# Kernel tuning notes

Measured on AMD Instinct MI355X. Metric: run time of the kernel, lower is better.

Reference implementation:

```python
import jax, jax.numpy as jnp
import numpy as np

B, T, D = 2, 2048, 2048
H, DH, DR, DL = 16, 128, 64, 512
WINDOW, STRIDE, GLOBAL = 512, 64, 128
BASE, MAX_SEQ, ORIG_MAX = 10000.0, 131072, 4096
BETA_FAST, BETA_SLOW = 32.0, 1.0
SCALE = 1.0 / np.sqrt(DH)
SCALE_ROPE = 1.0 / np.sqrt(DR)


def _yarn_inv_freq():
    base_inv = 1.0 / (BASE ** (np.arange(0, DR, 2, dtype=np.float32) / DR))
    scale = MAX_SEQ / ORIG_MAX
    freqs = np.arange(DR // 2, dtype=np.float32)
    ramp = np.clip((freqs - BETA_SLOW) / (BETA_FAST - BETA_SLOW), 0.0, 1.0)
    return jnp.asarray(base_inv * (1 - ramp) + (base_inv / scale) * ramp)

_INV_FREQ = _yarn_inv_freq()
_YARN_FACTOR = np.float32(0.1 * np.log(MAX_SEQ / ORIG_MAX) + 1.0)


def _apply_rope(x):
    # x: [B, H, T, DR]
    t = jnp.arange(x.shape[2], dtype=jnp.float32)
    fr = t[:, None] * _INV_FREQ[None, :]            # [T, DR/2]
    emb = jnp.concatenate([fr, fr], axis=-1)        # [T, DR]
    cos, sin = jnp.cos(emb), jnp.sin(emb)
    x1, x2 = jnp.split(x, 2, axis=-1)
    rot = jnp.concatenate([-x2, x1], axis=-1)
    return (x * cos + rot * sin) * _YARN_FACTOR


def _sparse_mask(seq_len):
    pos = jnp.arange(seq_len)
    qp, kp = pos[:, None], pos[None, :]
    dist = qp - kp
    half = WINDOW // 2
    window = (dist >= -half) & (dist <= half)
    dilated = (kp % STRIDE == 0) | (kp < GLOBAL)
    causal = kp <= qp
    return (window | dilated) & causal              # [T, T] bool


def setup_inputs() -> dict:
    key = jax.random.key(0)
    ks = jax.random.split(key, 9)
    s = 0.02
    return {
        "x": jax.random.normal(ks[0], (B, T, D), jnp.float32),
        "w_q": jax.random.normal(ks[1], (D, D), jnp.float32) * s,
        "w_dkv": jax.random.normal(ks[2], (D, DL), jnp.float32) * s,
        "w_uk": jax.random.normal(ks[3], (DL, D), jnp.float32) * s,
        "w_uv": jax.random.normal(ks[4], (DL, D), jnp.float32) * s,
        "w_q_pos": jax.random.normal(ks[5], (D, H * DR), jnp.float32) * s,
        "w_k_pos": jax.random.normal(ks[6], (D, H * DR), jnp.float32) * s,
        "w_o": jax.random.normal(ks[7], (D, D), jnp.float32) * s,
    }


def reference(x, w_q, w_dkv, w_uk, w_uv, w_q_pos, w_k_pos, w_o):
    b, t, _ = x.shape
    # MLA projections
    q_c = (x @ w_q).reshape(b, t, H, DH).transpose(0, 2, 1, 3)      # [B,H,T,DH]
    c_kv = x @ w_dkv                                                # [B,T,DL]
    k_c = (c_kv @ w_uk).reshape(b, t, H, DH).transpose(0, 2, 1, 3)
    v_c = (c_kv @ w_uv).reshape(b, t, H, DH).transpose(0, 2, 1, 3)
    # decoupled RoPE branch (YaRN)
    q_r = (x @ w_q_pos).reshape(b, t, H, DR).transpose(0, 2, 1, 3)
    k_r = (x @ w_k_pos).reshape(b, t, H, DR).transpose(0, 2, 1, 3)
    q_r = _apply_rope(q_r)
    k_r = _apply_rope(k_r)
    # combined content + positional scores
    scores = jnp.einsum("bhqd,bhkd->bhqk", q_c, k_c) * SCALE \
           + jnp.einsum("bhqr,bhkr->bhqk", q_r, k_r) * SCALE_ROPE
    mask = _sparse_mask(t)                                          # [T,T]
    scores = jnp.where(mask[None, None], scores, -jnp.inf)
    attn = jax.nn.softmax(scores, axis=-1)
    out = jnp.einsum("bhqk,bhkd->bhqd", attn, v_c)                  # [B,H,T,DH]
    out = out.transpose(0, 2, 1, 3).reshape(b, t, D)
    return out @ w_o
```

## Files before the change

kernel.cpp:

```cpp
#include <hip/hip_runtime.h>
#include <hip/hip_bf16.h>
#include <cstdint>

typedef __attribute__((ext_vector_type(8))) short short8_t;
typedef __attribute__((ext_vector_type(4))) short short4_t;
typedef __attribute__((ext_vector_type(4))) float f32x4_t;

#define AS1 __attribute__((address_space(1)))
#define AS3 __attribute__((address_space(3)))

__device__ __forceinline__ void gload_lds16(const void* g, void* l) {
  __builtin_amdgcn_global_load_lds((const AS1 void*)g, (AS3 void*)l, 16, 0, 0);
}

__device__ __forceinline__ short8_t ld8(const __hip_bfloat16* p) {
  return *(const short8_t*)p;
}

__global__ __launch_bounds__(256) void k_prep(
    const float* __restrict__ x, __hip_bfloat16* __restrict__ xb,
    const float* __restrict__ wq,  const float* __restrict__ wqp,
    const float* __restrict__ wkp, const float* __restrict__ wdkv,
    const float* __restrict__ wuk, const float* __restrict__ wuv,
    const float* __restrict__ wo,
    __hip_bfloat16* __restrict__ Bt1, __hip_bfloat16* __restrict__ Bt2,
    __hip_bfloat16* __restrict__ woT) {
  __shared__ float t[64][65];
  int bid = blockIdx.x;
  if (bid < 4096) {
    int i = (bid * 256 + threadIdx.x) * 8;
    union { short8_t v; __hip_bfloat16 h[8]; } u;
#pragma unroll
    for (int j = 0; j < 8; ++j) u.h[j] = __float2bfloat16(x[i + j]);
    *(short8_t*)(xb + i) = u.v;
    return;
  }
  bid -= 4096;
  const float* in; __hip_bfloat16* out; int R, C, tile;
  if (bid < 1024)      { in = wq;   out = Bt1;                 R = 2048; C = 2048; tile = bid; }
  else if (bid < 1536) { in = wqp;  out = Bt1 + 2048UL * 2048; R = 2048; C = 1024; tile = bid - 1024; }
  else if (bid < 2048) { in = wkp;  out = Bt1 + 3072UL * 2048; R = 2048; C = 1024; tile = bid - 1536; }
  else if (bid < 2304) { in = wdkv; out = Bt1 + 4096UL * 2048; R = 2048; C = 512;  tile = bid - 2048; }
  else if (bid < 2560) { in = wuk;  out = Bt2;                 R = 512;  C = 2048; tile = bid - 2304; }
  else if (bid < 2816) { in = wuv;  out = Bt2 + 2048UL * 512;  R = 512;  C = 2048; tile = bid - 2560; }
  else                 { in = wo;   out = woT;                 R = 2048; C = 2048; tile = bid - 2816; }
  int nct = C >> 6;
  int ct = tile % nct, rt = tile / nct;
  int r0 = rt << 6, c0 = ct << 6;
#pragma unroll
  for (int i = 0; i < 16; ++i) {
    int idx = i * 256 + threadIdx.x;
    int r = idx >> 6, c = idx & 63;
    t[r][c] = in[(size_t)(r0 + r) * C + c0 + c];
  }
  __syncthreads();
#pragma unroll
  for (int i = 0; i < 16; ++i) {
    int idx = i * 256 + threadIdx.x;
    int c = idx >> 6, r = idx & 63;
    out[(size_t)(c0 + c) * R + r0 + r] = __float2bfloat16(t[r][c]);
  }
}

template<int MODE>
__global__ __launch_bounds__(256) void k_gemm2(const __hip_bfloat16* __restrict__ A,
                                               const __hip_bfloat16* __restrict__ Bt,
                                               int K, int nbx,
                                               void* __restrict__ O0, void* __restrict__ O1,
                                               void* __restrict__ O2, void* __restrict__ O3,
                                               float alpha) {
  __shared__ __align__(16) __hip_bfloat16 Al[3][128 * 32];
  __shared__ __align__(16) __hip_bfloat16 Bl[3][128 * 32];
  int bx = blockIdx.x % nbx, by = blockIdx.x / nbx;
  int tid = threadIdx.x, lane = tid & 63, w = tid >> 6;
  int L = lane & 15, hi = lane >> 4;
  int wr = (w >> 1) << 6, wc = (w & 1) << 6;
  f32x4_t acc[4][4] = {};
  const __hip_bfloat16* Ag = A + (size_t)(by * 128) * K;
  const __hip_bfloat16* Bg = Bt + (size_t)(bx * 128) * K;
  int rA = w * 16 + (lane >> 2);
  int cA = ((lane & 3) ^ ((lane >> 3) & 3)) * 8;
  int NT = K >> 5;

  auto stage = [&](int s) {
    int j = s % 3;
    int k0 = s << 5;
    gload_lds16(Ag + (size_t)rA * K + k0 + cA,        &Al[j][(w * 16) * 32]);
    gload_lds16(Ag + (size_t)(rA + 64) * K + k0 + cA, &Al[j][(64 + w * 16) * 32]);
    gload_lds16(Bg + (size_t)rA * K + k0 + cA,        &Bl[j][(w * 16) * 32]);
    gload_lds16(Bg + (size_t)(rA + 64) * K + k0 + cA, &Bl[j][(64 + w * 16) * 32]);
  };

  stage(0); stage(1);
  asm volatile("s_waitcnt vmcnt(4)\ns_barrier" ::: "memory");

  int hs = hi ^ ((L >> 1) & 3);
  for (int t = 0; t < NT; ++t) {
    int j = t % 3;
    short8_t af[4], bf[4];
#pragma unroll
    for (int m = 0; m < 4; ++m) af[m] = ld8(&Al[j][(wr + 16 * m + L) * 32 + 8 * hs]);
#pragma unroll
    for (int n = 0; n < 4; ++n) bf[n] = ld8(&Bl[j][(wc + 16 * n + L) * 32 + 8 * hs]);
    if (t + 2 < NT) stage(t + 2);
    __builtin_amdgcn_s_setprio(1);
#pragma unroll
    for (int m = 0; m < 4; ++m)
#pragma unroll
      for (int n = 0; n < 4; ++n)
        acc[m][n] = __builtin_amdgcn_mfma_f32_16x16x32_bf16(af[m], bf[n], acc[m][n], 0, 0, 0);
    __builtin_amdgcn_s_setprio(0);
    if (t + 2 < NT)      asm volatile("s_waitcnt vmcnt(4)\ns_barrier" ::: "memory");
    else if (t + 1 < NT) asm volatile("s_waitcnt vmcnt(0)\ns_barrier" ::: "memory");
  }

  int r0 = by * 128 + wr + 4 * hi;
  int cb = bx * 128 + wc;

  if (MODE == 1) {
    float* C = (float*)O0;
    size_t N = (size_t)nbx << 7;
#pragma unroll
    for (int m = 0; m < 4; ++m)
#pragma unroll
      for (int n = 0; n < 4; ++n)
#pragma unroll
        for (int i = 0; i < 4; ++i)
          C[(size_t)(r0 + 16 * m + i) * N + cb + 16 * n + L] = acc[m][n][i] * alpha;
  } else if (MODE == 2) {
    __hip_bfloat16* qcb = (__hip_bfloat16*)O0;
    __hip_bfloat16* qrb = (__hip_bfloat16*)O1;
    __hip_bfloat16* krb = (__hip_bfloat16*)O2;
    __hip_bfloat16* ckv = (__hip_bfloat16*)O3;
    if (bx < 16) {
      const float SCALE = 0.08838834764831845f;
#pragma unroll
      for (int m = 0; m < 4; ++m)
#pragma unroll
        for (int n = 0; n < 4; ++n)
#pragma unroll
          for (int i = 0; i < 4; ++i)
            qcb[(size_t)(r0 + 16 * m + i) * 2048 + cb + 16 * n + L] =
                __float2bfloat16(acc[m][n][i] * SCALE);
    } else if (bx < 32) {
      bool isq = bx < 24;
      __hip_bfloat16* dst = isq ? qrb : krb;
      float osc = isq ? 0.16832169878499666f : 1.3465735902799727f;
      int cbl = cb - (isq ? 2048 : 3072);
      float invf[2];
#pragma unroll
      for (int p = 0; p < 2; ++p) {
        float fi = (float)(16 * p + L);
        float bi = __expf(fi * -0.28782313662425574f);
        float ramp = fminf(fmaxf((fi - 1.0f) * (1.0f / 31.0f), 0.0f), 1.0f);
        invf[p] = bi * (1.0f - ramp * (31.0f / 32.0f));
      }
#pragma unroll
      for (int m = 0; m < 4; ++m)
#pragma unroll
        for (int i = 0; i < 4; ++i) {
          int row = r0 + 16 * m + i;
          float ft = (float)(row & 2047);
#pragma unroll
          for (int p = 0; p < 2; ++p) {
            float sn, cs;
            __sincosf(ft * invf[p], &sn, &cs);
            float x1 = acc[m][p][i], x2 = acc[m][p + 2][i];
            dst[(size_t)row * 1024 + cbl + 16 * p + L] =
                __float2bfloat16((x1 * cs - x2 * sn) * osc);
            dst[(size_t)row * 1024 + cbl + 32 + 16 * p + L] =
                __float2bfloat16((x2 * cs + x1 * sn) * osc);
          }
        }
    } else {
      int cbl = cb - 4096;
#pragma unroll
      for (int m = 0; m < 4; ++m)
#pragma unroll
        for (int n = 0; n < 4; ++n)
#pragma unroll
          for (int i = 0; i < 4; ++i)
            ckv[(size_t)(r0 + 16 * m + i) * 512 + cbl + 16 * n + L] =
                __float2bfloat16(acc[m][n][i]);
    }
  } else if (MODE == 3) {
    __hip_bfloat16* kcb = (__hip_bfloat16*)O0;
    __hip_bfloat16* vcb = (__hip_bfloat16*)O1;
    __hip_bfloat16* vT  = (__hip_bfloat16*)O2;
    if (bx < 16) {
#pragma unroll
      for (int m = 0; m < 4; ++m)
#pragma unroll
        for (int n = 0; n < 4; ++n)
#pragma unroll
          for (int i = 0; i < 4; ++i)
            kcb[(size_t)(r0 + 16 * m + i) * 2048 + cb + 16 * n + L] =
                __float2bfloat16(acc[m][n][i]);
    } else {
#pragma unroll
      for (int m = 0; m < 4; ++m)
#pragma unroll
        for (int n = 0; n < 4; ++n) {
          int vcol = cb - 2048 + 16 * n + L;
          int hh = vcol >> 7, dh = vcol & 127;
          int row0 = r0 + 16 * m;
          int b = row0 >> 11, t0 = row0 & 2047;
          union { short4_t v; __hip_bfloat16 h4[4]; } pk;
#pragma unroll
          for (int i = 0; i < 4; ++i) {
            __hip_bfloat16 bv = __float2bfloat16(acc[m][n][i]);
            vcb[(size_t)(row0 + i) * 2048 + vcol] = bv;
            pk.h4[i] = bv;
          }
          *(short4_t*)(vT + ((size_t)((b * 16 + hh) * 128 + dh) * 2048 + t0)) = pk.v;
        }
    }
  }
}

__global__ __launch_bounds__(256) void k_attn(const __hip_bfloat16* __restrict__ qc,
                                              const __hip_bfloat16* __restrict__ kc,
                                              const __hip_bfloat16* __restrict__ vcb,
                                              const __hip_bfloat16* __restrict__ qr,
                                              const __hip_bfloat16* __restrict__ kr,
                                              const __hip_bfloat16* __restrict__ vT,
                                              __hip_bfloat16* __restrict__ ao) {
  const int T = 2048;
  int bid = blockIdx.x;
  int xcd = bid & 7, r = bid >> 3;
  int j = r >> 5, qt = r & 31;
  int bh = xcd + 8 * j;
  int b = bh >> 4, h = bh & 15;
  int tid = threadIdx.x, lane = tid & 63, w = tid >> 6;
  int L = lane & 15, hi = lane >> 4;
  int q0 = qt * 64;

  __shared__ __align__(16) __hip_bfloat16 Kl[64 * 200];
  __shared__ __align__(16) __hip_bfloat16 Vt[128 * 64];
  __shared__ __align__(16) __hip_bfloat16 Pl[4][16 * 72];

  char* Vtb = (char*)Vt;
  const __hip_bfloat16* vTb = vT + (size_t)(b * 16 + h) * 128 * 2048;

  int qrow = q0 + w * 16 + L;
  size_t qb = (size_t)b * T + qrow;
  short8_t qf[6];
#pragma unroll
  for (int c = 0; c < 4; ++c)
    qf[c] = ld8(qc + qb * 2048 + h * 128 + 32 * c + 8 * hi);
#pragma unroll
  for (int c = 0; c < 2; ++c)
    qf[4 + c] = ld8(qr + qb * 1024 + h * 64 + 32 * c + 8 * hi);

  f32x4_t oacc[8] = {};
  float mrow[4], lrow[4];
#pragma unroll
  for (int i = 0; i < 4; ++i) { mrow[i] = -1e30f; lrow[i] = 0.0f; }

  int nd = qt - 6;

  for (int step = 0; step <= qt + 1; ++step) {
    bool compact = (step == qt + 1);
    if (compact && nd <= 0) break;
    int kt = step;
    if (!compact && kt > 1 && kt < qt - 4) continue;
    int k0 = kt * 64;

    if (!compact) {
#pragma unroll
      for (int i = 0; i < 6; ++i) {
        int ch = i * 256 + tid;
        int rr = ch / 24;
        int d = (ch % 24) * 8;
        size_t krow = (size_t)b * T + k0 + rr;
        const __hip_bfloat16* src = (d < 128)
            ? kc + krow * 2048 + h * 128 + d
            : kr + krow * 1024 + h * 64 + (d - 128);
        *(short8_t*)(Kl + rr * 200 + d) = ld8(src);
      }
#pragma unroll
      for (int i = 0; i < 4; ++i) {
        int ch = i * 256 + tid;
        int row = ch >> 3, c = ch & 7;
        int swc = c ^ (row & 7);
        *(short8_t*)(Vtb + row * 128 + 16 * swc) = ld8(vTb + (size_t)row * 2048 + k0 + c * 8);
      }
    } else {
#pragma unroll
      for (int i = 0; i < 6; ++i) {
        int ch = i * 256 + tid;
        int rr = ch / 24;
        int d = (ch % 24) * 8;
        int srcr = (rr < nd) ? 64 * (2 + rr) : 0;
        size_t krow = (size_t)b * T + srcr;
        const __hip_bfloat16* src = (d < 128)
            ? kc + krow * 2048 + h * 128 + d
            : kr + krow * 1024 + h * 64 + (d - 128);
        *(short8_t*)(Kl + rr * 200 + d) = ld8(src);
      }
#pragma unroll
      for (int i = 0; i < 2; ++i) {
        int ch = i * 256 + tid;
        int jj = ch >> 4, d0 = (ch & 15) * 8;
        if (jj < nd) {
          union { short8_t v; __hip_bfloat16 hh[8]; } u;
          u.v = ld8(vcb + (size_t)(b * 2048 + 64 * (2 + jj)) * 2048 + h * 128 + d0);
#pragma unroll
          for (int qq = 0; qq < 8; ++qq) {
            int dh = d0 + qq;
            int swc = (jj >> 3) ^ (dh & 7);
            *(__hip_bfloat16*)(Vtb + dh * 128 + 16 * swc + 2 * (jj & 7)) = u.hh[qq];
          }
        }
      }
    }
    __syncthreads();

    f32x4_t sacc[4] = {};
    __builtin_amdgcn_s_setprio(1);
#pragma unroll
    for (int n = 0; n < 4; ++n)
#pragma unroll
      for (int c = 0; c < 6; ++c) {
        short8_t bfr = ld8(Kl + (16 * n + L) * 200 + 32 * c + 8 * hi);
        sacc[n] = __builtin_amdgcn_mfma_f32_16x16x32_bf16(qf[c], bfr, sacc[n], 0, 0, 0);
      }
    __builtin_amdgcn_s_setprio(0);

    int rbase = q0 + w * 16 + 4 * hi;
    float p[4][4];
    float mt[4];
#pragma unroll
    for (int i = 0; i < 4; ++i) mt[i] = -1e30f;
#pragma unroll
    for (int n = 0; n < 4; ++n) {
      int col = L + 16 * n;
      int k = k0 + col;
#pragma unroll
      for (int i = 0; i < 4; ++i) {
        int rq = rbase + i;
        bool ok = compact ? (col < nd)
                          : ((k <= rq) && ((rq - k <= 256) || ((k & 63) == 0) || (k < 128)));
        float s = ok ? sacc[n][i] : -1e30f;
        p[n][i] = s;
        mt[i] = fmaxf(mt[i], s);
      }
    }
    for (int d = 1; d < 16; d <<= 1)
#pragma unroll
      for (int i = 0; i < 4; ++i) mt[i] = fmaxf(mt[i], __shfl_xor(mt[i], d, 64));
    float al[4], rs[4];
#pragma unroll
    for (int i = 0; i < 4; ++i) {
      float mnew = fmaxf(mrow[i], mt[i]);
      al[i] = __expf(mrow[i] - mnew);
      mrow[i] = mnew;
      rs[i] = 0.0f;
    }
#pragma unroll
    for (int n = 0; n < 4; ++n)
#pragma unroll
      for (int i = 0; i < 4; ++i) {
        float e = __expf(p[n][i] - mrow[i]);
        p[n][i] = e;
        rs[i] += e;
      }
    for (int d = 1; d < 16; d <<= 1)
#pragma unroll
      for (int i = 0; i < 4; ++i) rs[i] += __shfl_xor(rs[i], d, 64);
#pragma unroll
    for (int i = 0; i < 4; ++i) lrow[i] = lrow[i] * al[i] + rs[i];
#pragma unroll
    for (int n = 0; n < 8; ++n)
#pragma unroll
      for (int i = 0; i < 4; ++i) oacc[n][i] *= al[i];

#pragma unroll
    for (int n = 0; n < 4; ++n)
#pragma unroll
      for (int i = 0; i < 4; ++i)
        Pl[w][(4 * hi + i) * 72 + 16 * n + L] = __float2bfloat16(p[n][i]);
    __syncthreads();

    __builtin_amdgcn_s_setprio(1);
#pragma unroll
    for (int ks = 0; ks < 2; ++ks) {
      short8_t pa = ld8(Pl[w] + L * 72 + 32 * ks + 8 * hi);
#pragma unroll
      for (int n = 0; n < 8; ++n) {
        int vrow = 16 * n + L;
        int chunk = (4 * ks + hi) ^ (vrow & 7);
        short8_t bv = *(const short8_t*)(Vtb + vrow * 128 + 16 * chunk);
        oacc[n] = __builtin_amdgcn_mfma_f32_16x16x32_bf16(pa, bv, oacc[n], 0, 0, 0);
      }
    }
    __builtin_amdgcn_s_setprio(0);
    __syncthreads();
  }

#pragma unroll
  for (int n = 0; n < 8; ++n)
#pragma unroll
    for (int i = 0; i < 4; ++i) {
      int rq = q0 + w * 16 + 4 * hi + i;
      int cdh = 16 * n + L;
      float v = oacc[n][i] / lrow[i];
      ao[((size_t)b * T + rq) * 2048 + h * 128 + cdh] = __float2bfloat16(v);
    }
}

extern "C" void kernel_launch(void* const* d_in, const int* in_sizes, int n_in,
                              void* d_out, int out_size, void* d_ws, size_t ws_size,
                              hipStream_t stream) {
  const float* x     = (const float*)d_in[0];
  const float* w_q   = (const float*)d_in[1];
  const float* w_dkv = (const float*)d_in[2];
  const float* w_uk  = (const float*)d_in[3];
  const float* w_uv  = (const float*)d_in[4];
  const float* w_qp  = (const float*)d_in[5];
  const float* w_kp  = (const float*)d_in[6];
  const float* w_o   = (const float*)d_in[7];
  float* out = (float*)d_out;

  char* ws = (char*)d_ws;
  size_t off = 0;
  auto alloc = [&](size_t elems) {
    __hip_bfloat16* p = (__hip_bfloat16*)(ws + off);
    off += ((elems * 2 + 255) & ~(size_t)255);
    return p;
  };
  __hip_bfloat16* xb  = alloc(8388608);
  __hip_bfloat16* Bt1 = alloc(4608UL * 2048);
  __hip_bfloat16* Bt2 = alloc(4096UL * 512);
  __hip_bfloat16* woT = alloc(4194304);
  __hip_bfloat16* qcb = alloc(8388608);
  __hip_bfloat16* ckv = alloc(2097152);
  __hip_bfloat16* kcb = alloc(8388608);
  __hip_bfloat16* vcb = alloc(8388608);
  __hip_bfloat16* qrb = alloc(4194304);
  __hip_bfloat16* krb = alloc(4194304);
  __hip_bfloat16* aob = alloc(8388608);
  __hip_bfloat16* vT  = alloc(8388608);

  k_prep<<<7936, 256, 0, stream>>>(x, xb, w_q, w_qp, w_kp, w_dkv, w_uk, w_uv, w_o,
                                   Bt1, Bt2, woT);

  k_gemm2<2><<<36 * 32, 256, 0, stream>>>(xb, Bt1, 2048, 36, qcb, qrb, krb, ckv, 1.0f);
  k_gemm2<3><<<32 * 32, 256, 0, stream>>>(ckv, Bt2, 512, 32, kcb, vcb, vT, nullptr, 1.0f);

  k_attn<<<1024, 256, 0, stream>>>(qcb, kcb, vcb, qrb, krb, vT, aob);

  k_gemm2<1><<<16 * 32, 256, 0, stream>>>(aob, woT, 2048, 16, out, nullptr, nullptr, nullptr, 1.0f);
}
```

Measured before the change: 268.5 us.

## Use 256-row GEMM tiles and prefetch next K/V tile in attention

The projection GEMMs switch to a 512-thread kernel with 256x128 output tiles, so each B tile is reused across more rows and fewer blocks are launched. The attention kernel now precomputes its list of key tiles and loads the next tile's K/V into registers while the current tile is being computed, overlapping global loads with MFMA work. It also drops the barrier after the per-wave P write, since each wave only reads its own P buffer. This costs more registers and may lower occupancy, and the larger GEMM tiles may leave the grid less balanced.

```diff
diff --git a/kernel.cpp b/kernel.cpp
--- a/kernel.cpp
+++ b/kernel.cpp
@@ -62,13 +62,10 @@
   }
 }
 
-template<int MODE>
-__global__ __launch_bounds__(256) void k_gemm2(const __hip_bfloat16* __restrict__ A,
-                                               const __hip_bfloat16* __restrict__ Bt,
-                                               int K, int nbx,
-                                               void* __restrict__ O0, void* __restrict__ O1,
-                                               void* __restrict__ O2, void* __restrict__ O3,
-                                               float alpha) {
+__global__ __launch_bounds__(256) void k_gemm_s(const __hip_bfloat16* __restrict__ A,
+                                                const __hip_bfloat16* __restrict__ Bt,
+                                                int K, int nbx, float* __restrict__ C,
+                                                float alpha) {
   __shared__ __align__(16) __hip_bfloat16 Al[3][128 * 32];
   __shared__ __align__(16) __hip_bfloat16 Bl[3][128 * 32];
   int bx = blockIdx.x % nbx, by = blockIdx.x / nbx;
@@ -115,19 +112,72 @@
   }
 
   int r0 = by * 128 + wr + 4 * hi;
+  int c0 = bx * 128 + wc;
+  size_t N = (size_t)nbx << 7;
+#pragma unroll
+  for (int m = 0; m < 4; ++m)
+#pragma unroll
+    for (int n = 0; n < 4; ++n)
+#pragma unroll
+      for (int i = 0; i < 4; ++i)
+        C[(size_t)(r0 + 16 * m + i) * N + c0 + 16 * n + L] = acc[m][n][i] * alpha;
+}
+
+template<int MODE>
+__global__ __launch_bounds__(512) void k_gemm_b(const __hip_bfloat16* __restrict__ A,
+                                                const __hip_bfloat16* __restrict__ Bt,
+                                                int K, int nbx,
+                                                void* __restrict__ O0, void* __restrict__ O1,
+                                                void* __restrict__ O2, void* __restrict__ O3) {
+  __shared__ __align__(16) __hip_bfloat16 Al[3][256 * 32];
+  __shared__ __align__(16) __hip_bfloat16 Bl[3][128 * 32];
+  int bx = blockIdx.x % nbx, by = blockIdx.x / nbx;
+  int tid = threadIdx.x, lane = tid & 63, w = tid >> 6;
+  int L = lane & 15, hi = lane >> 4;
+  int wr = (w >> 1) << 6;
+  int wc = (w & 1) << 6;
+  f32x4_t acc[4][4] = {};
+  const __hip_bfloat16* Ag = A + (size_t)(by * 256) * K;
+  const __hip_bfloat16* Bg = Bt + (size_t)(bx * 128) * K;
+  int rA = w * 16 + (lane >> 2);
+  int cA = ((lane & 3) ^ ((lane >> 3) & 3)) * 8;
+  int NT = K >> 5;
+
+  auto stage = [&](int s) {
+    int j = s % 3;
+    int k0 = s << 5;
+    gload_lds16(Ag + (size_t)rA * K + k0 + cA,         &Al[j][(w * 16) * 32]);
+    gload_lds16(Ag + (size_t)(rA + 128) * K + k0 + cA, &Al[j][(128 + w * 16) * 32]);
+    gload_lds16(Bg + (size_t)rA * K + k0 + cA,         &Bl[j][(w * 16) * 32]);
+  };
+
+  stage(0); stage(1);
+  asm volatile("s_waitcnt vmcnt(3)\ns_barrier" ::: "memory");
+
+  int hs = hi ^ ((L >> 1) & 3);
+  for (int t = 0; t < NT; ++t) {
+    int j = t % 3;
+    short8_t af[4], bf[4];
+#pragma unroll
+    for (int m = 0; m < 4; ++m) af[m] = ld8(&Al[j][(wr + 16 * m + L) * 32 + 8 * hs]);
+#pragma unroll
+    for (int n = 0; n < 4; ++n) bf[n] = ld8(&Bl[j][(wc + 16 * n + L) * 32 + 8 * hs]);
+    if (t + 2 < NT) stage(t + 2);
+    __builtin_amdgcn_s_setprio(1);
+#pragma unroll
+    for (int m = 0; m < 4; ++m)
+#pragma unroll
+      for (int n = 0; n < 4; ++n)
+        acc[m][n] = __builtin_amdgcn_mfma_f32_16x16x32_bf16(af[m], bf[n], acc[m][n], 0, 0, 0);
+    __builtin_amdgcn_s_setprio(0);
+    if (t + 2 < NT)      asm volatile("s_waitcnt vmcnt(3)\ns_barrier" ::: "memory");
+    else if (t + 1 < NT) asm volatile("s_waitcnt vmcnt(0)\ns_barrier" ::: "memory");
+  }
+
+  int r0 = by * 256 + wr + 4 * hi;
   int cb = bx * 128 + wc;
 
-  if (MODE == 1) {
-    float* C = (float*)O0;
-    size_t N = (size_t)nbx << 7;
-#pragma unroll
-    for (int m = 0; m < 4; ++m)
-#pragma unroll
-      for (int n = 0; n < 4; ++n)
-#pragma unroll
-        for (int i = 0; i < 4; ++i)
-          C[(size_t)(r0 + 16 * m + i) * N + cb + 16 * n + L] = acc[m][n][i] * alpha;
-  } else if (MODE == 2) {
+  if (MODE == 2) {
     __hip_bfloat16* qcb = (__hip_bfloat16*)O0;
     __hip_bfloat16* qrb = (__hip_bfloat16*)O1;
     __hip_bfloat16* krb = (__hip_bfloat16*)O2;
@@ -227,9 +277,9 @@
                                               __hip_bfloat16* __restrict__ ao) {
   const int T = 2048;
   int bid = blockIdx.x;
-  int xcd = bid & 7, r = bid >> 3;
-  int j = r >> 5, qt = r & 31;
-  int bh = xcd + 8 * j;
+  int xcd = bid & 7, rr0 = bid >> 3;
+  int jj0 = rr0 >> 5, qt = rr0 & 31;
+  int bh = xcd + 8 * jj0;
   int b = bh >> 4, h = bh & 15;
   int tid = threadIdx.x, lane = tid & 63, w = tid >> 6;
   int L = lane & 15, hi = lane >> 4;
@@ -259,52 +309,71 @@
 
   int nd = qt - 6;
 
-  for (int step = 0; step <= qt + 1; ++step) {
-    bool compact = (step == qt + 1);
-    if (compact && nd <= 0) break;
-    int kt = step;
-    if (!compact && kt > 1 && kt < qt - 4) continue;
-    int k0 = kt * 64;
-
-    if (!compact) {
-#pragma unroll
-      for (int i = 0; i < 6; ++i) {
+  int k0s[9]; int ns = 0;
+  if (qt <= 6) {
+    for (int s = 0; s <= qt; ++s) k0s[ns++] = s * 64;
+  } else {
+    k0s[ns++] = 0; k0s[ns++] = 64;
+    for (int s = qt - 4; s <= qt; ++s) k0s[ns++] = s * 64;
+    if (nd > 0) k0s[ns++] = -1;
+  }
+
+  short8_t kpre[6], vpre[4];
+
+  auto loadKV = [&](int idx) {
+    bool cp = (k0s[idx] < 0);
+    int k0 = cp ? 0 : k0s[idx];
+#pragma unroll
+    for (int i = 0; i < 6; ++i) {
+      int ch = i * 256 + tid;
+      int r = ch / 24, d = (ch % 24) * 8;
+      int srcr = cp ? ((r < nd) ? 64 * (2 + r) : 0) : (k0 + r);
+      size_t krow = (size_t)b * T + srcr;
+      kpre[i] = (d < 128) ? ld8(kc + krow * 2048 + h * 128 + d)
+                          : ld8(kr + krow * 1024 + h * 64 + (d - 128));
+    }
+    if (!cp) {
+#pragma unroll
+      for (int i = 0; i < 4; ++i) {
         int ch = i * 256 + tid;
-        int rr = ch / 24;
-        int d = (ch % 24) * 8;
-        size_t krow = (size_t)b * T + k0 + rr;
-        const __hip_bfloat16* src = (d < 128)
-            ? kc + krow * 2048 + h * 128 + d
-            : kr + krow * 1024 + h * 64 + (d - 128);
-        *(short8_t*)(Kl + rr * 200 + d) = ld8(src);
-      }
+        int row = ch >> 3, c = ch & 7;
+        vpre[i] = ld8(vTb + (size_t)row * 2048 + k0 + c * 8);
+      }
+    } else {
+#pragma unroll
+      for (int i = 0; i < 2; ++i) {
+        int ch = i * 256 + tid;
+        int jj = ch >> 4, d0 = (ch & 15) * 8;
+        int jje = (jj < nd) ? jj : 0;
+        vpre[i] = ld8(vcb + (size_t)(b * 2048 + 64 * (2 + jje)) * 2048 + h * 128 + d0);
+      }
+    }
+  };
+
+  auto writeKV = [&](int idx) {
+    bool cp = (k0s[idx] < 0);
+#pragma unroll
+    for (int i = 0; i < 6; ++i) {
+      int ch = i * 256 + tid;
+      int r = ch / 24, d = (ch % 24) * 8;
+      *(short8_t*)(Kl + r * 200 + d) = kpre[i];
+    }
+    if (!cp) {
 #pragma unroll
       for (int i = 0; i < 4; ++i) {
         int ch = i * 256 + tid;
         int row = ch >> 3, c = ch & 7;
         int swc = c ^ (row & 7);
-        *(short8_t*)(Vtb + row * 128 + 16 * swc) = ld8(vTb + (size_t)row * 2048 + k0 + c * 8);
+        *(short8_t*)(Vtb + row * 128 + 16 * swc) = vpre[i];
       }
     } else {
-#pragma unroll
-      for (int i = 0; i < 6; ++i) {
-        int ch = i * 256 + tid;
-        int rr = ch / 24;
-        int d = (ch % 24) * 8;
-        int srcr = (rr < nd) ? 64 * (2 + rr) : 0;
-        size_t krow = (size_t)b * T + srcr;
-        const __hip_bfloat16* src = (d < 128)
-            ? kc + krow * 2048 + h * 128 + d
-            : kr + krow * 1024 + h * 64 + (d - 128);
-        *(short8_t*)(Kl + rr * 200 + d) = ld8(src);
-      }
 #pragma unroll
       for (int i = 0; i < 2; ++i) {
         int ch = i * 256 + tid;
         int jj = ch >> 4, d0 = (ch & 15) * 8;
         if (jj < nd) {
           union { short8_t v; __hip_bfloat16 hh[8]; } u;
-          u.v = ld8(vcb + (size_t)(b * 2048 + 64 * (2 + jj)) * 2048 + h * 128 + d0);
+          u.v = vpre[i];
 #pragma unroll
           for (int qq = 0; qq < 8; ++qq) {
             int dh = d0 + qq;
@@ -314,7 +383,17 @@
         }
       }
     }
+  };
+
+  loadKV(0);
+
+  for (int it = 0; it < ns; ++it) {
+    bool compact = (k0s[it] < 0);
+    int k0 = compact ? 0 : k0s[it];
+
+    writeKV(it);
     __syncthreads();
+    if (it + 1 < ns) loadKV(it + 1);
 
     f32x4_t sacc[4] = {};
     __builtin_amdgcn_s_setprio(1);
@@ -380,7 +459,6 @@
 #pragma unroll
       for (int i = 0; i < 4; ++i)
         Pl[w][(4 * hi + i) * 72 + 16 * n + L] = __float2bfloat16(p[n][i]);
-    __syncthreads();
 
     __builtin_amdgcn_s_setprio(1);
 #pragma unroll
@@ -445,10 +523,10 @@
   k_prep<<<7936, 256, 0, stream>>>(x, xb, w_q, w_qp, w_kp, w_dkv, w_uk, w_uv, w_o,
                                    Bt1, Bt2, woT);
 
-  k_gemm2<2><<<36 * 32, 256, 0, stream>>>(xb, Bt1, 2048, 36, qcb, qrb, krb, ckv, 1.0f);
-  k_gemm2<3><<<32 * 32, 256, 0, stream>>>(ckv, Bt2, 512, 32, kcb, vcb, vT, nullptr, 1.0f);
+  k_gemm_b<2><<<36 * 16, 512, 0, stream>>>(xb, Bt1, 2048, 36, qcb, qrb, krb, ckv);
+  k_gemm_b<3><<<32 * 16, 512, 0, stream>>>(ckv, Bt2, 512, 32, kcb, vcb, vT, nullptr);
 
   k_attn<<<1024, 256, 0, stream>>>(qcb, kcb, vcb, qrb, krb, vT, aob);
 
-  k_gemm2<1><<<16 * 32, 256, 0, stream>>>(aob, woT, 2048, 16, out, nullptr, nullptr, nullptr, 1.0f);
-}
+  k_gemm_s<<<16 * 32, 256, 0, stream>>>(aob, woT, 2048, 16, out, 1.0f);
+}
```

Result: slower. 313.8 us (+16.9%).

## Split attention key tiles across two blocks and merge partials in a combine kernel

Applied to the files above, without the earlier changes.

Each query tile's list of key tiles is now split into two halves, each processed by its own block (grid doubles to 2048). Each block writes an unnormalised bf16 partial output plus per-row max and sum. A new combine kernel merges the two partials with log-sum-exp weights and normalises them. The goal is more parallelism and better load balance across CUs. The cost is an extra kernel launch, an extra read and write pass over partial outputs, bf16 rounding of the unnormalised partials, and scratch space taken from reused workspace buffers (xb, Bt2).

```diff
diff --git a/kernel.cpp b/kernel.cpp
--- a/kernel.cpp
+++ b/kernel.cpp
@@ -218,18 +218,21 @@
   }
 }
 
-__global__ __launch_bounds__(256) void k_attn(const __hip_bfloat16* __restrict__ qc,
-                                              const __hip_bfloat16* __restrict__ kc,
-                                              const __hip_bfloat16* __restrict__ vcb,
-                                              const __hip_bfloat16* __restrict__ qr,
-                                              const __hip_bfloat16* __restrict__ kr,
-                                              const __hip_bfloat16* __restrict__ vT,
-                                              __hip_bfloat16* __restrict__ ao) {
+__global__ __launch_bounds__(256) void k_attn_part(const __hip_bfloat16* __restrict__ qc,
+                                                   const __hip_bfloat16* __restrict__ kc,
+                                                   const __hip_bfloat16* __restrict__ vcb,
+                                                   const __hip_bfloat16* __restrict__ qr,
+                                                   const __hip_bfloat16* __restrict__ kr,
+                                                   const __hip_bfloat16* __restrict__ vT,
+                                                   __hip_bfloat16* __restrict__ po,
+                                                   float* __restrict__ ml) {
   const int T = 2048;
   int bid = blockIdx.x;
   int xcd = bid & 7, r = bid >> 3;
-  int j = r >> 5, qt = r & 31;
-  int bh = xcd + 8 * j;
+  int qt = r & 31;
+  int half = (r >> 5) & 1;
+  int jg = r >> 6;
+  int bh = xcd + 8 * jg;
   int b = bh >> 4, h = bh & 15;
   int tid = threadIdx.x, lane = tid & 63, w = tid >> 6;
   int L = lane & 15, hi = lane >> 4;
@@ -259,12 +262,21 @@
 
   int nd = qt - 6;
 
-  for (int step = 0; step <= qt + 1; ++step) {
-    bool compact = (step == qt + 1);
-    if (compact && nd <= 0) break;
-    int kt = step;
-    if (!compact && kt > 1 && kt < qt - 4) continue;
-    int k0 = kt * 64;
+  int k0s[9]; int ns = 0;
+  if (qt <= 6) {
+    for (int s = 0; s <= qt; ++s) k0s[ns++] = s * 64;
+  } else {
+    k0s[ns++] = 0; k0s[ns++] = 64;
+    for (int s = qt - 4; s <= qt; ++s) k0s[ns++] = s * 64;
+    if (nd > 0) k0s[ns++] = -1;
+  }
+  int h0 = (ns + 1) >> 1;
+  int ibeg = half ? h0 : 0;
+  int iend = half ? ns : h0;
+
+  for (int it = ibeg; it < iend; ++it) {
+    bool compact = (k0s[it] < 0);
+    int k0 = compact ? 0 : k0s[it];
 
     if (!compact) {
 #pragma unroll
@@ -398,15 +410,48 @@
     __syncthreads();
   }
 
+  __hip_bfloat16* pod = po + (size_t)half * 8388608;
 #pragma unroll
   for (int n = 0; n < 8; ++n)
 #pragma unroll
     for (int i = 0; i < 4; ++i) {
       int rq = q0 + w * 16 + 4 * hi + i;
       int cdh = 16 * n + L;
-      float v = oacc[n][i] / lrow[i];
-      ao[((size_t)b * T + rq) * 2048 + h * 128 + cdh] = __float2bfloat16(v);
-    }
+      pod[((size_t)b * T + rq) * 2048 + h * 128 + cdh] = __float2bfloat16(oacc[n][i]);
+    }
+  if (L == 0) {
+#pragma unroll
+    for (int i = 0; i < 4; ++i) {
+      int rq = q0 + w * 16 + 4 * hi + i;
+      size_t o = (((size_t)half * 4096 + b * 2048 + rq) * 16 + h) * 2;
+      ml[o] = mrow[i];
+      ml[o + 1] = lrow[i];
+    }
+  }
+}
+
+__global__ __launch_bounds__(256) void k_combine(const __hip_bfloat16* __restrict__ po,
+                                                 const float* __restrict__ ml,
+                                                 __hip_bfloat16* __restrict__ ao) {
+  int idx = blockIdx.x * 256 + threadIdx.x;
+  int row = idx >> 8;
+  int col = (idx & 255) * 8;
+  int h = col >> 7;
+  size_t mo = ((size_t)row * 16 + h) * 2;
+  float m1 = ml[mo],                    l1 = ml[mo + 1];
+  float m2 = ml[mo + 4096 * 16 * 2],    l2 = ml[mo + 4096 * 16 * 2 + 1];
+  float m = fmaxf(m1, m2);
+  float w1 = __expf(m1 - m), w2 = __expf(m2 - m);
+  float inv = 1.0f / (w1 * l1 + w2 * l2);
+  size_t o = (size_t)row * 2048 + col;
+  union { short8_t v; __hip_bfloat16 h8[8]; } a, bb, c;
+  a.v = *(const short8_t*)(po + o);
+  bb.v = *(const short8_t*)(po + 8388608 + o);
+#pragma unroll
+  for (int j = 0; j < 8; ++j)
+    c.h8[j] = __float2bfloat16(
+        (w1 * __bfloat162float(a.h8[j]) + w2 * __bfloat162float(bb.h8[j])) * inv);
+  *(short8_t*)(ao + o) = c.v;
 }
 
 extern "C" void kernel_launch(void* const* d_in, const int* in_sizes, int n_in,
@@ -448,7 +493,11 @@
   k_gemm2<2><<<36 * 32, 256, 0, stream>>>(xb, Bt1, 2048, 36, qcb, qrb, krb, ckv, 1.0f);
   k_gemm2<3><<<32 * 32, 256, 0, stream>>>(ckv, Bt2, 512, 32, kcb, vcb, vT, nullptr, 1.0f);
 
-  k_attn<<<1024, 256, 0, stream>>>(qcb, kcb, vcb, qrb, krb, vT, aob);
+  __hip_bfloat16* po  = xb;
+  float*          mlp = (float*)Bt2;
+
+  k_attn_part<<<2048, 256, 0, stream>>>(qcb, kcb, vcb, qrb, krb, vT, po, mlp);
+  k_combine<<<4096, 256, 0, stream>>>(po, mlp, aob);
 
   k_gemm2<1><<<16 * 32, 256, 0, stream>>>(aob, woT, 2048, 16, out, nullptr, nullptr, nullptr, 1.0f);
 }
```

New measurement: 273.2 us. About the same (+1.8%).

## Process 128 queries per attention block with 8 waves sharing K/V tiles

Applied to the files above, without the earlier changes.

The attention kernel now launches 512 blocks of 512 threads. Each block covers two adjacent 64-query tiles, so every K/V tile staged in shared memory is reused by twice as many waves, which halves global K/V loading per query. The list of key tiles to visit (global, window and compacted dilated keys) is built up front in a small array. A block-wide barrier between writing and reading the per-wave P buffer is removed, since each wave only touches its own slice. The cost is that the lower-half waves also process the extra diagonal tile and must mask it entirely. Larger blocks also carry more shared memory and register pressure, which may lower occupancy.

```diff
diff --git a/kernel.cpp b/kernel.cpp
--- a/kernel.cpp
+++ b/kernel.cpp
@@ -218,26 +218,27 @@
   }
 }
 
-__global__ __launch_bounds__(256) void k_attn(const __hip_bfloat16* __restrict__ qc,
-                                              const __hip_bfloat16* __restrict__ kc,
-                                              const __hip_bfloat16* __restrict__ vcb,
-                                              const __hip_bfloat16* __restrict__ qr,
-                                              const __hip_bfloat16* __restrict__ kr,
-                                              const __hip_bfloat16* __restrict__ vT,
-                                              __hip_bfloat16* __restrict__ ao) {
+__global__ __launch_bounds__(512, 4) void k_attn(const __hip_bfloat16* __restrict__ qc,
+                                                 const __hip_bfloat16* __restrict__ kc,
+                                                 const __hip_bfloat16* __restrict__ vcb,
+                                                 const __hip_bfloat16* __restrict__ qr,
+                                                 const __hip_bfloat16* __restrict__ kr,
+                                                 const __hip_bfloat16* __restrict__ vT,
+                                                 __hip_bfloat16* __restrict__ ao) {
   const int T = 2048;
   int bid = blockIdx.x;
   int xcd = bid & 7, r = bid >> 3;
-  int j = r >> 5, qt = r & 31;
-  int bh = xcd + 8 * j;
+  int qp = r & 15;
+  int jg = r >> 4;
+  int bh = xcd + 8 * jg;
   int b = bh >> 4, h = bh & 15;
   int tid = threadIdx.x, lane = tid & 63, w = tid >> 6;
   int L = lane & 15, hi = lane >> 4;
-  int q0 = qt * 64;
+  int q0 = qp * 128;
 
   __shared__ __align__(16) __hip_bfloat16 Kl[64 * 200];
   __shared__ __align__(16) __hip_bfloat16 Vt[128 * 64];
-  __shared__ __align__(16) __hip_bfloat16 Pl[4][16 * 72];
+  __shared__ __align__(16) __hip_bfloat16 Pl[8][16 * 72];
 
   char* Vtb = (char*)Vt;
   const __hip_bfloat16* vTb = vT + (size_t)(b * 16 + h) * 128 * 2048;
@@ -257,19 +258,22 @@
 #pragma unroll
   for (int i = 0; i < 4; ++i) { mrow[i] = -1e30f; lrow[i] = 0.0f; }
 
-  int nd = qt - 6;
-
-  for (int step = 0; step <= qt + 1; ++step) {
-    bool compact = (step == qt + 1);
-    if (compact && nd <= 0) break;
-    int kt = step;
-    if (!compact && kt > 1 && kt < qt - 4) continue;
-    int k0 = kt * 64;
+  int nd = 2 * qp - 6;
+
+  int k0s[10]; int ns = 0;
+  int last = 2 * qp + 1;
+  for (int s = 0; s <= last; ++s)
+    if (s <= 1 || s >= 2 * qp - 4) k0s[ns++] = s * 64;
+  if (nd > 0) k0s[ns++] = -1;
+
+  for (int it = 0; it < ns; ++it) {
+    bool compact = (k0s[it] < 0);
+    int k0 = compact ? 0 : k0s[it];
 
     if (!compact) {
 #pragma unroll
-      for (int i = 0; i < 6; ++i) {
-        int ch = i * 256 + tid;
+      for (int i = 0; i < 3; ++i) {
+        int ch = i * 512 + tid;
         int rr = ch / 24;
         int d = (ch % 24) * 8;
         size_t krow = (size_t)b * T + k0 + rr;
@@ -279,16 +283,16 @@
         *(short8_t*)(Kl + rr * 200 + d) = ld8(src);
       }
 #pragma unroll
-      for (int i = 0; i < 4; ++i) {
-        int ch = i * 256 + tid;
+      for (int i = 0; i < 2; ++i) {
+        int ch = i * 512 + tid;
         int row = ch >> 3, c = ch & 7;
         int swc = c ^ (row & 7);
         *(short8_t*)(Vtb + row * 128 + 16 * swc) = ld8(vTb + (size_t)row * 2048 + k0 + c * 8);
       }
     } else {
 #pragma unroll
-      for (int i = 0; i < 6; ++i) {
-        int ch = i * 256 + tid;
+      for (int i = 0; i < 3; ++i) {
+        int ch = i * 512 + tid;
         int rr = ch / 24;
         int d = (ch % 24) * 8;
         int srcr = (rr < nd) ? 64 * (2 + rr) : 0;
@@ -298,9 +302,8 @@
             : kr + krow * 1024 + h * 64 + (d - 128);
         *(short8_t*)(Kl + rr * 200 + d) = ld8(src);
       }
-#pragma unroll
-      for (int i = 0; i < 2; ++i) {
-        int ch = i * 256 + tid;
+      {
+        int ch = tid;
         int jj = ch >> 4, d0 = (ch & 15) * 8;
         if (jj < nd) {
           union { short8_t v; __hip_bfloat16 hh[8]; } u;
@@ -380,7 +383,6 @@
 #pragma unroll
       for (int i = 0; i < 4; ++i)
         Pl[w][(4 * hi + i) * 72 + 16 * n + L] = __float2bfloat16(p[n][i]);
-    __syncthreads();
 
     __builtin_amdgcn_s_setprio(1);
 #pragma unroll
@@ -448,7 +450,7 @@
   k_gemm2<2><<<36 * 32, 256, 0, stream>>>(xb, Bt1, 2048, 36, qcb, qrb, krb, ckv, 1.0f);
   k_gemm2<3><<<32 * 32, 256, 0, stream>>>(ckv, Bt2, 512, 32, kcb, vcb, vT, nullptr, 1.0f);
 
-  k_attn<<<1024, 256, 0, stream>>>(qcb, kcb, vcb, qrb, krb, vT, aob);
+  k_attn<<<512, 512, 0, stream>>>(qcb, kcb, vcb, qrb, krb, vT, aob);
 
   k_gemm2<1><<<16 * 32, 256, 0, stream>>>(aob, woT, 2048, 16, out, nullptr, nullptr, nullptr, 1.0f);
 }
```

Result: slower. 288.2 us (+7.3%).
